# Kernel optimization log

Measured on AMD Instinct MI355X. Metric: run time of the kernel, lower is better.

Reference implementation:

```python
import jax, jax.numpy as jnp
import numpy as np

B, E, H, NF, NO, L = 1024, 256, 4, 16384, 49152, 192
DH = E // H
NEG = -1e9  # effectively -inf for masked-out padded keys


def _positions(batch, n, offset_counts=None):
    # batch is sorted; within-segment index = i - segment_start[batch[i]]
    counts = jax.ops.segment_sum(jnp.ones((n,), jnp.int32), batch, num_segments=B)
    start = jnp.cumsum(counts) - counts
    pos = jnp.arange(n, dtype=jnp.int32) - start[batch]
    if offset_counts is not None:
        pos = pos + offset_counts[batch]
    return pos, counts


def setup_inputs() -> dict:
    key = jax.random.key(0)
    ks = jax.random.split(key, 8)
    scene_feat = jax.random.normal(ks[0], (B, E), jnp.float32)
    face_nodes = jax.random.normal(ks[1], (NF, E), jnp.float32)
    obj_nodes = jax.random.normal(ks[2], (NO, E), jnp.float32)
    face_batch = jnp.sort(jax.random.randint(ks[3], (NF,), 0, B))
    obj_batch = jnp.sort(jax.random.randint(ks[4], (NO,), 0, B))
    s = 1.0 / np.sqrt(E)
    in_proj_w = jax.random.uniform(ks[5], (3 * E, E), jnp.float32, -s, s)
    in_proj_b = jnp.zeros((3 * E,), jnp.float32)
    out_proj_w = jax.random.uniform(ks[6], (E, E), jnp.float32, -s, s)
    out_proj_b = jnp.zeros((E,), jnp.float32)
    ln_gamma = jnp.ones((E,), jnp.float32)
    ln_beta = jnp.zeros((E,), jnp.float32)
    return dict(scene_feat=scene_feat, face_nodes=face_nodes, obj_nodes=obj_nodes,
                face_batch=face_batch, obj_batch=obj_batch,
                in_proj_w=in_proj_w, in_proj_b=in_proj_b,
                out_proj_w=out_proj_w, out_proj_b=out_proj_b,
                ln_gamma=ln_gamma, ln_beta=ln_beta)


def reference(scene_feat, face_nodes, obj_nodes, face_batch, obj_batch,
              in_proj_w, in_proj_b, out_proj_w, out_proj_b, ln_gamma, ln_beta):
    # --- to_dense_batch over concat([face, obj]) : faces first per graph ---
    pos_f, counts_f = _positions(face_batch, NF)
    pos_o, _ = _positions(obj_batch, NO, offset_counts=counts_f)
    all_nodes = jnp.concatenate([face_nodes, obj_nodes], axis=0)   # [N, E]
    all_batch = jnp.concatenate([face_batch, obj_batch], axis=0)   # [N]
    all_pos = jnp.concatenate([pos_f, pos_o], axis=0)              # [N]
    slot = jnp.where(all_pos < L, all_pos, L)                      # overflow -> sentinel col
    dense = jnp.zeros((B, L + 1, E), all_nodes.dtype).at[all_batch, slot].set(all_nodes)[:, :L]
    mask = jnp.zeros((B, L + 1), bool).at[all_batch, slot].set(True)[:, :L]

    # --- single-query multihead cross-attention (torch MHA semantics) ---
    wq, wk, wv = in_proj_w[:E], in_proj_w[E:2 * E], in_proj_w[2 * E:]
    bq, bk, bv = in_proj_b[:E], in_proj_b[E:2 * E], in_proj_b[2 * E:]
    q = (scene_feat @ wq.T + bq).reshape(B, H, DH)                 # [B,H,DH]
    k = (dense @ wk.T + bk).reshape(B, L, H, DH)
    v = (dense @ wv.T + bv).reshape(B, L, H, DH)
    scores = jnp.einsum('bhd,blhd->bhl', q, k) / np.sqrt(DH)        # [B,H,L]
    scores = jnp.where(mask[:, None, :], scores, NEG)
    attn = jax.nn.softmax(scores, axis=-1)                          # [B,H,L]
    ctx = jnp.einsum('bhl,blhd->bhd', attn, v).reshape(B, E)
    attn_out = ctx @ out_proj_w.T + out_proj_b                      # [B,E]

    # --- residual + LayerNorm ---
    x = scene_feat + attn_out
    mu = jnp.mean(x, axis=-1, keepdims=True)
    var = jnp.mean(jnp.square(x - mu), axis=-1, keepdims=True)
    fused = (x - mu) * jax.lax.rsqrt(var + 1e-5) * ln_gamma + ln_beta  # [B,E]

    attn_weights = jnp.mean(attn, axis=1)[:, None, :]               # [B,1,L] head-averaged
    return fused, attn_weights
```

## Files before the change

### kernel.cpp

```cpp
#include <hip/hip_runtime.h>
#include <math.h>

#define B 1024
#define E 256
#define H 4
#define DH 64
#define L 192
#define NF 16384
#define NO 49152
#define BPB 4

__global__ __launch_bounds__(256) void prep_kernel(
    const int* __restrict__ fb, const int* __restrict__ ob,
    int* __restrict__ start_f, int* __restrict__ start_o,
    const float* __restrict__ ipw, const float* __restrict__ opw,
    float* __restrict__ WT)
{
  int blk = blockIdx.x;
  if (blk < 192) {
    int m = blk / 64;
    int r = blk % 64;
    int bx = (r & 7) * 32, by = (r >> 3) * 32;
    const float* src = (m == 0) ? ipw : (m == 1 ? ipw + 2 * E * E : opw);
    float* dst = WT + (size_t)m * E * E;
    __shared__ float tile[32][33];
    int tx = threadIdx.x & 31, ty = threadIdx.x >> 5;
#pragma unroll
    for (int i = 0; i < 32; i += 8)
      tile[ty + i][tx] = src[(size_t)(by + ty + i) * E + bx + tx];
    __syncthreads();
#pragma unroll
    for (int i = 0; i < 32; i += 8)
      dst[(size_t)(bx + ty + i) * E + by + tx] = tile[tx][ty + i];
  } else {
    int b = (blk - 192) * 256 + threadIdx.x;
    if (b > B) return;
    int lo = 0, hi = NF;
    while (lo < hi) { int m = (lo + hi) >> 1; if (fb[m] < b) lo = m + 1; else hi = m; }
    start_f[b] = lo;
    lo = 0; hi = NO;
    while (lo < hi) { int m = (lo + hi) >> 1; if (ob[m] < b) lo = m + 1; else hi = m; }
    start_o[b] = lo;
  }
}

__global__ __launch_bounds__(512, 2) void fused_kernel(
    const float* __restrict__ scene,
    const float* __restrict__ face, const float* __restrict__ obj,
    const float* __restrict__ ipw, const float* __restrict__ ipb,
    const float* __restrict__ WqT, const float* __restrict__ WvT,
    const float* __restrict__ WoT, const float* __restrict__ opb,
    const float* __restrict__ gamma, const float* __restrict__ beta,
    const int* __restrict__ start_f, const int* __restrict__ start_o,
    float* __restrict__ fusedO, float* __restrict__ attnw)
{
  int b0 = blockIdx.x * BPB;
  int t = threadIdx.x, wave = t >> 6, lane = t & 63;

  __shared__ float sc_s[BPB][E];
  __shared__ float q_s[BPB][E];
  __shared__ float Y_s[BPB][H][E];
  __shared__ float Z_s[BPB][H][E];
  __shared__ float ctx_s[BPB][E];
  __shared__ float s_s[BPB][H][L];
  __shared__ float part_s[8][BPB][E];
  __shared__ float Zp_s[BPB][2][H][E];
  __shared__ float mw_s[BPB][2][H], su_s[BPB][2][H], sb_s[BPB][H];
  __shared__ int   info_s[BPB][4];

  for (int i = t; i < BPB * E; i += 512)
    ((float*)sc_s)[i] = scene[(size_t)b0 * E + i];
  if (t < BPB) {
    int b = b0 + t;
    int sf0 = start_f[b], cf = start_f[b + 1] - sf0;
    int so0 = start_o[b], co = start_o[b + 1] - so0;
    info_s[t][0] = sf0; info_s[t][1] = so0;
    info_s[t][2] = min(cf, L); info_s[t][3] = min(cf + co, L);
  }
  __syncthreads();

  {
    const float4* W4 = (const float4*)WqT + lane;
    float4 a0 = {0,0,0,0}, a1 = {0,0,0,0}, a2 = {0,0,0,0}, a3 = {0,0,0,0};
    int j0 = wave * 32;
#pragma unroll
    for (int jj = 0; jj < 32; ++jj) {
      int j = j0 + jj;
      float4 w = W4[(size_t)j * 64];
      float s0 = sc_s[0][j], s1 = sc_s[1][j], s2 = sc_s[2][j], s3 = sc_s[3][j];
      a0.x += s0*w.x; a0.y += s0*w.y; a0.z += s0*w.z; a0.w += s0*w.w;
      a1.x += s1*w.x; a1.y += s1*w.y; a1.z += s1*w.z; a1.w += s1*w.w;
      a2.x += s2*w.x; a2.y += s2*w.y; a2.z += s2*w.z; a2.w += s2*w.w;
      a3.x += s3*w.x; a3.y += s3*w.y; a3.z += s3*w.z; a3.w += s3*w.w;
    }
    *(float4*)&part_s[wave][0][4 * lane] = a0;
    *(float4*)&part_s[wave][1][4 * lane] = a1;
    *(float4*)&part_s[wave][2][4 * lane] = a2;
    *(float4*)&part_s[wave][3][4 * lane] = a3;
  }
  __syncthreads();
  for (int i = t; i < BPB * E; i += 512) {
    int bi = i >> 8, e = i & 255;
    float v = ipb[e];
#pragma unroll
    for (int w = 0; w < 8; ++w) v += part_s[w][bi][e];
    q_s[bi][e] = v;
  }
  __syncthreads();

  if (wave < BPB) {
#pragma unroll
    for (int h = 0; h < H; ++h) {
      float v = q_s[wave][h * DH + lane] * ipb[E + h * DH + lane];
#pragma unroll
      for (int o = 32; o; o >>= 1) v += __shfl_xor(v, o);
      if (lane == 0) sb_s[wave][h] = v;
    }
  }

  {
    const float* Wk = ipw + (size_t)E * E;
    int h = wave >> 1, d0 = (wave & 1) * 32;
    float4 a0 = {0,0,0,0}, a1 = {0,0,0,0}, a2 = {0,0,0,0}, a3 = {0,0,0,0};
#pragma unroll
    for (int dd = 0; dd < 32; ++dd) {
      int d = d0 + dd;
      float4 w = *((const float4*)(Wk + (size_t)(h * DH + d) * E) + lane);
      float q0 = q_s[0][h * DH + d], q1 = q_s[1][h * DH + d];
      float q2 = q_s[2][h * DH + d], q3 = q_s[3][h * DH + d];
      a0.x += q0*w.x; a0.y += q0*w.y; a0.z += q0*w.z; a0.w += q0*w.w;
      a1.x += q1*w.x; a1.y += q1*w.y; a1.z += q1*w.z; a1.w += q1*w.w;
      a2.x += q2*w.x; a2.y += q2*w.y; a2.z += q2*w.z; a2.w += q2*w.w;
      a3.x += q3*w.x; a3.y += q3*w.y; a3.z += q3*w.z; a3.w += q3*w.w;
    }
    float* Yp = (float*)part_s;
    int wi = wave & 1;
    size_t o0 = (((size_t)wi * BPB + 0) * H + h) * E + 4 * lane;
    size_t o1 = (((size_t)wi * BPB + 1) * H + h) * E + 4 * lane;
    size_t o2 = (((size_t)wi * BPB + 2) * H + h) * E + 4 * lane;
    size_t o3 = (((size_t)wi * BPB + 3) * H + h) * E + 4 * lane;
    *(float4*)&Yp[o0] = a0; *(float4*)&Yp[o1] = a1;
    *(float4*)&Yp[o2] = a2; *(float4*)&Yp[o3] = a3;
  }
  __syncthreads();
  {
    float* Yp = (float*)part_s;
    for (int i = t; i < BPB * H * E; i += 512)
      ((float*)Y_s)[i] = Yp[i] + Yp[BPB * H * E + i];
  }
  __syncthreads();

  {
    int bb = wave >> 1, wi = wave & 1;
    int g = lane >> 4, sl = lane & 15;
    int sf0 = info_s[bb][0], so0 = info_s[bb][1];
    int n_f = info_s[bb][2], n = info_s[bb][3];

    float4 y[H][4];
#pragma unroll
    for (int h = 0; h < H; ++h)
#pragma unroll
      for (int k = 0; k < 4; ++k)
        y[h][k] = *(const float4*)&Y_s[bb][h][4 * (sl + 16 * k)];
    float sbv[H];
#pragma unroll
    for (int h = 0; h < H; ++h) sbv[h] = sb_s[bb][h];

    float m[H] = {-3.0e38f, -3.0e38f, -3.0e38f, -3.0e38f};
    float u[H] = {0.f, 0.f, 0.f, 0.f};
    float4 acc[H][4] = {};

    int s0 = wi * 4 + g;
    float4 x[4] = {};
    if (s0 < n) {
      const float* xr = (s0 < n_f) ? face + (size_t)(sf0 + s0) * E
                                   : obj  + (size_t)(so0 + s0 - n_f) * E;
#pragma unroll
      for (int k = 0; k < 4; ++k) x[k] = ((const float4*)xr)[sl + 16 * k];
    }

    for (int s = s0; s < n; s += 8) {
      float4 xn[4] = {};
      int sn = s + 8;
      if (sn < n) {
        const float* xr = (sn < n_f) ? face + (size_t)(sf0 + sn) * E
                                     : obj  + (size_t)(so0 + sn - n_f) * E;
#pragma unroll
        for (int k = 0; k < 4; ++k) xn[k] = ((const float4*)xr)[sl + 16 * k];
      }

      float p[H];
#pragma unroll
      for (int h = 0; h < H; ++h) {
        float a = 0.f;
#pragma unroll
        for (int k = 0; k < 4; ++k)
          a += x[k].x * y[h][k].x + x[k].y * y[h][k].y +
               x[k].z * y[h][k].z + x[k].w * y[h][k].w;
        p[h] = a;
      }
#pragma unroll
      for (int off = 8; off; off >>= 1) {
#pragma unroll
        for (int h = 0; h < H; ++h) p[h] += __shfl_xor(p[h], off);
      }
#pragma unroll
      for (int h = 0; h < H; ++h) p[h] = (p[h] + sbv[h]) * 0.125f;
      if (sl == 0) {
#pragma unroll
        for (int h = 0; h < H; ++h) s_s[bb][h][s] = p[h];
      }
#pragma unroll
      for (int h = 0; h < H; ++h) {
        if (p[h] > m[h]) {
          float f = __expf(m[h] - p[h]);
#pragma unroll
          for (int k = 0; k < 4; ++k) {
            acc[h][k].x = acc[h][k].x * f + x[k].x;
            acc[h][k].y = acc[h][k].y * f + x[k].y;
            acc[h][k].z = acc[h][k].z * f + x[k].z;
            acc[h][k].w = acc[h][k].w * f + x[k].w;
          }
          u[h] = u[h] * f + 1.f;
          m[h] = p[h];
        } else {
          float e = __expf(p[h] - m[h]);
#pragma unroll
          for (int k = 0; k < 4; ++k) {
            acc[h][k].x += e * x[k].x;
            acc[h][k].y += e * x[k].y;
            acc[h][k].z += e * x[k].z;
            acc[h][k].w += e * x[k].w;
          }
          u[h] += e;
        }
      }
#pragma unroll
      for (int k = 0; k < 4; ++k) x[k] = xn[k];
    }

#pragma unroll
    for (int off = 16; off <= 32; off <<= 1) {
#pragma unroll
      for (int h = 0; h < H; ++h) {
        float mo = __shfl_xor(m[h], off);
        float uo = __shfl_xor(u[h], off);
        float M = fmaxf(m[h], mo);
        float fs = __expf(m[h] - M), fo = __expf(mo - M);
        u[h] = fs * u[h] + fo * uo;
        m[h] = M;
#pragma unroll
        for (int k = 0; k < 4; ++k) {
          float ax = __shfl_xor(acc[h][k].x, off);
          float ay = __shfl_xor(acc[h][k].y, off);
          float az = __shfl_xor(acc[h][k].z, off);
          float aw = __shfl_xor(acc[h][k].w, off);
          acc[h][k].x = fs * acc[h][k].x + fo * ax;
          acc[h][k].y = fs * acc[h][k].y + fo * ay;
          acc[h][k].z = fs * acc[h][k].z + fo * az;
          acc[h][k].w = fs * acc[h][k].w + fo * aw;
        }
      }
    }
    if (g == 0) {
#pragma unroll
      for (int h = 0; h < H; ++h)
#pragma unroll
        for (int k = 0; k < 4; ++k)
          *(float4*)&Zp_s[bb][wi][h][4 * (sl + 16 * k)] = acc[h][k];
    }
    if (lane == 0) {
#pragma unroll
      for (int h = 0; h < H; ++h) {
        mw_s[bb][wi][h] = m[h];
        su_s[bb][wi][h] = u[h];
      }
    }
  }
  __syncthreads();

  for (int i = t; i < BPB * H * E; i += 512) {
    int bi = i >> 10, rem = i & 1023, h = rem >> 8, e = rem & 255;
    float z = 0.f;
    if (info_s[bi][3] > 0) {
      float ma = mw_s[bi][0][h], mb = mw_s[bi][1][h];
      float M = fmaxf(ma, mb);
      float fa = __expf(ma - M), fb = __expf(mb - M);
      float inv = 1.0f / (fa * su_s[bi][0][h] + fb * su_s[bi][1][h]);
      z = (fa * Zp_s[bi][0][h][e] + fb * Zp_s[bi][1][h][e]) * inv;
    }
    ((float*)Z_s)[i] = z;
  }
  for (int i = t; i < BPB * L; i += 512) {
    int bi = i / L, s = i - bi * L;
    int n = info_s[bi][3];
    float v;
    if (n == 0) v = 1.0f / L;
    else if (s < n) {
      v = 0.f;
#pragma unroll
      for (int h = 0; h < H; ++h) {
        float ma = mw_s[bi][0][h], mb = mw_s[bi][1][h];
        float M = fmaxf(ma, mb);
        float fa = __expf(ma - M), fb = __expf(mb - M);
        float inv = 1.0f / (fa * su_s[bi][0][h] + fb * su_s[bi][1][h]);
        v += __expf(s_s[bi][h][s] - M) * inv;
      }
      v *= 0.25f;
    } else v = 0.f;
    attnw[(size_t)(b0 + bi) * L + s] = v;
  }
  __syncthreads();

  {
    const float4* W4 = (const float4*)WvT + lane;
    int j0 = wave * 32, hoff = (lane >> 4) * E;
    float4 a0 = {0,0,0,0}, a1 = {0,0,0,0}, a2 = {0,0,0,0}, a3 = {0,0,0,0};
#pragma unroll
    for (int jj = 0; jj < 32; ++jj) {
      int j = j0 + jj;
      float4 w = W4[(size_t)j * 64];
      float z0 = ((float*)Z_s[0])[hoff + j];
      float z1 = ((float*)Z_s[1])[hoff + j];
      float z2 = ((float*)Z_s[2])[hoff + j];
      float z3 = ((float*)Z_s[3])[hoff + j];
      a0.x += z0*w.x; a0.y += z0*w.y; a0.z += z0*w.z; a0.w += z0*w.w;
      a1.x += z1*w.x; a1.y += z1*w.y; a1.z += z1*w.z; a1.w += z1*w.w;
      a2.x += z2*w.x; a2.y += z2*w.y; a2.z += z2*w.z; a2.w += z2*w.w;
      a3.x += z3*w.x; a3.y += z3*w.y; a3.z += z3*w.z; a3.w += z3*w.w;
    }
    *(float4*)&part_s[wave][0][4 * lane] = a0;
    *(float4*)&part_s[wave][1][4 * lane] = a1;
    *(float4*)&part_s[wave][2][4 * lane] = a2;
    *(float4*)&part_s[wave][3][4 * lane] = a3;
  }
  __syncthreads();
  for (int i = t; i < BPB * E; i += 512) {
    int bi = i >> 8, e = i & 255;
    float v = ipb[2 * E + e];
#pragma unroll
    for (int w = 0; w < 8; ++w) v += part_s[w][bi][e];
    ctx_s[bi][e] = v;
  }
  __syncthreads();

  {
    const float4* W4 = (const float4*)WoT + lane;
    int j0 = wave * 32;
    float4 a0 = {0,0,0,0}, a1 = {0,0,0,0}, a2 = {0,0,0,0}, a3 = {0,0,0,0};
#pragma unroll
    for (int jj = 0; jj < 32; ++jj) {
      int j = j0 + jj;
      float4 w = W4[(size_t)j * 64];
      float c0 = ctx_s[0][j], c1 = ctx_s[1][j], c2 = ctx_s[2][j], c3 = ctx_s[3][j];
      a0.x += c0*w.x; a0.y += c0*w.y; a0.z += c0*w.z; a0.w += c0*w.w;
      a1.x += c1*w.x; a1.y += c1*w.y; a1.z += c1*w.z; a1.w += c1*w.w;
      a2.x += c2*w.x; a2.y += c2*w.y; a2.z += c2*w.z; a2.w += c2*w.w;
      a3.x += c3*w.x; a3.y += c3*w.y; a3.z += c3*w.z; a3.w += c3*w.w;
    }
    *(float4*)&part_s[wave][0][4 * lane] = a0;
    *(float4*)&part_s[wave][1][4 * lane] = a1;
    *(float4*)&part_s[wave][2][4 * lane] = a2;
    *(float4*)&part_s[wave][3][4 * lane] = a3;
  }
  __syncthreads();
  for (int i = t; i < BPB * E; i += 512) {
    int bi = i >> 8, e = i & 255;
    float v = opb[e] + sc_s[bi][e];
#pragma unroll
    for (int w = 0; w < 8; ++w) v += part_s[w][bi][e];
    q_s[bi][e] = v;
  }
  __syncthreads();

  if (wave < BPB) {
    float v0 = q_s[wave][lane], v1 = q_s[wave][lane + 64],
          v2 = q_s[wave][lane + 128], v3 = q_s[wave][lane + 192];
    float s1 = v0 + v1 + v2 + v3;
#pragma unroll
    for (int o = 32; o; o >>= 1) s1 += __shfl_xor(s1, o);
    float mu = s1 * (1.0f / E);
    float d0 = v0 - mu, d1 = v1 - mu, d2 = v2 - mu, d3 = v3 - mu;
    float s2 = d0*d0 + d1*d1 + d2*d2 + d3*d3;
#pragma unroll
    for (int o = 32; o; o >>= 1) s2 += __shfl_xor(s2, o);
    float inv = 1.0f / sqrtf(s2 * (1.0f / E) + 1e-5f);
    size_t base = (size_t)(b0 + wave) * E;
    fusedO[base + lane      ] = d0 * inv * gamma[lane      ] + beta[lane      ];
    fusedO[base + lane +  64] = d1 * inv * gamma[lane +  64] + beta[lane +  64];
    fusedO[base + lane + 128] = d2 * inv * gamma[lane + 128] + beta[lane + 128];
    fusedO[base + lane + 192] = d3 * inv * gamma[lane + 192] + beta[lane + 192];
  }
}

extern "C" void kernel_launch(void* const* d_in, const int* in_sizes, int n_in,
                              void* d_out, int out_size, void* d_ws, size_t ws_size,
                              hipStream_t stream) {
  const float* scene = (const float*)d_in[0];
  const float* face  = (const float*)d_in[1];
  const float* obj   = (const float*)d_in[2];
  const int*   fb    = (const int*)d_in[3];
  const int*   ob    = (const int*)d_in[4];
  const float* ipw   = (const float*)d_in[5];
  const float* ipb   = (const float*)d_in[6];
  const float* opw   = (const float*)d_in[7];
  const float* opb   = (const float*)d_in[8];
  const float* gam   = (const float*)d_in[9];
  const float* bet   = (const float*)d_in[10];

  float* fused = (float*)d_out;
  float* attnw = fused + (size_t)B * E;

  int* start_f = (int*)d_ws;
  int* start_o = start_f + (B + 1);
  float* WT   = (float*)((char*)d_ws + (16 << 10));
  float* WqT = WT;
  float* WvT = WT + (size_t)E * E;
  float* WoT = WT + (size_t)2 * E * E;

  prep_kernel<<<197, 256, 0, stream>>>(fb, ob, start_f, start_o, ipw, opw, WT);
  fused_kernel<<<B / BPB, 512, 0, stream>>>(scene, face, obj, ipw, ipb,
                                            WqT, WvT, WoT, opb, gam, bet,
                                            start_f, start_o, fused, attnw);
}
```

Before: 54.89 us.

## Split fused attention kernel into projection, per-batch streaming, and output kernels

The single fused kernel (4 batches per 512-thread block) is split into three kernels. qy_kernel computes q and the key-folded query Y. stream_kernel runs one 256-thread block per batch with 4 waves streaming that batch's node rows and merging their online-softmax partials. out_kernel applies the V and output projections plus LayerNorm. The aim is more parallelism in the memory-bound streaming phase, with four times as many blocks and smaller per-block shared memory, at the cost of two extra launches and global round-trips for Y and Z. The small GEMVs also drop their 4-batch register blocking, so each weight load is reused across fewer batches.

```diff
diff --git a/kernel.cpp b/kernel.cpp
--- a/kernel.cpp
+++ b/kernel.cpp
@@ -44,67 +44,42 @@
   }
 }
 
-__global__ __launch_bounds__(512, 2) void fused_kernel(
+__global__ __launch_bounds__(1024) void qy_kernel(
     const float* __restrict__ scene,
-    const float* __restrict__ face, const float* __restrict__ obj,
     const float* __restrict__ ipw, const float* __restrict__ ipb,
-    const float* __restrict__ WqT, const float* __restrict__ WvT,
-    const float* __restrict__ WoT, const float* __restrict__ opb,
-    const float* __restrict__ gamma, const float* __restrict__ beta,
-    const int* __restrict__ start_f, const int* __restrict__ start_o,
-    float* __restrict__ fusedO, float* __restrict__ attnw)
+    const float* __restrict__ WqT,
+    float* __restrict__ Yws, float* __restrict__ sbws)
 {
   int b0 = blockIdx.x * BPB;
   int t = threadIdx.x, wave = t >> 6, lane = t & 63;
+  int bw = wave >> 2, sub = wave & 3;
 
   __shared__ float sc_s[BPB][E];
   __shared__ float q_s[BPB][E];
-  __shared__ float Y_s[BPB][H][E];
-  __shared__ float Z_s[BPB][H][E];
-  __shared__ float ctx_s[BPB][E];
-  __shared__ float s_s[BPB][H][L];
-  __shared__ float part_s[8][BPB][E];
-  __shared__ float Zp_s[BPB][2][H][E];
-  __shared__ float mw_s[BPB][2][H], su_s[BPB][2][H], sb_s[BPB][H];
-  __shared__ int   info_s[BPB][4];
-
-  for (int i = t; i < BPB * E; i += 512)
-    ((float*)sc_s)[i] = scene[(size_t)b0 * E + i];
-  if (t < BPB) {
-    int b = b0 + t;
-    int sf0 = start_f[b], cf = start_f[b + 1] - sf0;
-    int so0 = start_o[b], co = start_o[b + 1] - so0;
-    info_s[t][0] = sf0; info_s[t][1] = so0;
-    info_s[t][2] = min(cf, L); info_s[t][3] = min(cf + co, L);
-  }
+  __shared__ float part_s[4][BPB][E];
+
+  sc_s[t >> 8][t & 255] = scene[(size_t)b0 * E + t];
   __syncthreads();
 
   {
     const float4* W4 = (const float4*)WqT + lane;
-    float4 a0 = {0,0,0,0}, a1 = {0,0,0,0}, a2 = {0,0,0,0}, a3 = {0,0,0,0};
-    int j0 = wave * 32;
-#pragma unroll
-    for (int jj = 0; jj < 32; ++jj) {
+    const float* sc = sc_s[bw];
+    float4 a = {0.f, 0.f, 0.f, 0.f};
+    int j0 = sub * 64;
+#pragma unroll 8
+    for (int jj = 0; jj < 64; ++jj) {
       int j = j0 + jj;
       float4 w = W4[(size_t)j * 64];
-      float s0 = sc_s[0][j], s1 = sc_s[1][j], s2 = sc_s[2][j], s3 = sc_s[3][j];
-      a0.x += s0*w.x; a0.y += s0*w.y; a0.z += s0*w.z; a0.w += s0*w.w;
-      a1.x += s1*w.x; a1.y += s1*w.y; a1.z += s1*w.z; a1.w += s1*w.w;
-      a2.x += s2*w.x; a2.y += s2*w.y; a2.z += s2*w.z; a2.w += s2*w.w;
-      a3.x += s3*w.x; a3.y += s3*w.y; a3.z += s3*w.z; a3.w += s3*w.w;
-    }
-    *(float4*)&part_s[wave][0][4 * lane] = a0;
-    *(float4*)&part_s[wave][1][4 * lane] = a1;
-    *(float4*)&part_s[wave][2][4 * lane] = a2;
-    *(float4*)&part_s[wave][3][4 * lane] = a3;
-  }
-  __syncthreads();
-  for (int i = t; i < BPB * E; i += 512) {
-    int bi = i >> 8, e = i & 255;
-    float v = ipb[e];
-#pragma unroll
-    for (int w = 0; w < 8; ++w) v += part_s[w][bi][e];
-    q_s[bi][e] = v;
+      float s = sc[j];
+      a.x += s * w.x; a.y += s * w.y; a.z += s * w.z; a.w += s * w.w;
+    }
+    *(float4*)&part_s[sub][bw][4 * lane] = a;
+  }
+  __syncthreads();
+  {
+    int bi = t >> 8, e = t & 255;
+    q_s[bi][e] = part_s[0][bi][e] + part_s[1][bi][e] +
+                 part_s[2][bi][e] + part_s[3][bi][e] + ipb[e];
   }
   __syncthreads();
 
@@ -114,268 +89,276 @@
       float v = q_s[wave][h * DH + lane] * ipb[E + h * DH + lane];
 #pragma unroll
       for (int o = 32; o; o >>= 1) v += __shfl_xor(v, o);
-      if (lane == 0) sb_s[wave][h] = v;
+      if (lane == 0) sbws[(size_t)(b0 + wave) * H + h] = v;
     }
   }
 
   {
     const float* Wk = ipw + (size_t)E * E;
-    int h = wave >> 1, d0 = (wave & 1) * 32;
-    float4 a0 = {0,0,0,0}, a1 = {0,0,0,0}, a2 = {0,0,0,0}, a3 = {0,0,0,0};
-#pragma unroll
-    for (int dd = 0; dd < 32; ++dd) {
-      int d = d0 + dd;
-      float4 w = *((const float4*)(Wk + (size_t)(h * DH + d) * E) + lane);
-      float q0 = q_s[0][h * DH + d], q1 = q_s[1][h * DH + d];
-      float q2 = q_s[2][h * DH + d], q3 = q_s[3][h * DH + d];
-      a0.x += q0*w.x; a0.y += q0*w.y; a0.z += q0*w.z; a0.w += q0*w.w;
-      a1.x += q1*w.x; a1.y += q1*w.y; a1.z += q1*w.z; a1.w += q1*w.w;
-      a2.x += q2*w.x; a2.y += q2*w.y; a2.z += q2*w.z; a2.w += q2*w.w;
-      a3.x += q3*w.x; a3.y += q3*w.y; a3.z += q3*w.z; a3.w += q3*w.w;
-    }
-    float* Yp = (float*)part_s;
-    int wi = wave & 1;
-    size_t o0 = (((size_t)wi * BPB + 0) * H + h) * E + 4 * lane;
-    size_t o1 = (((size_t)wi * BPB + 1) * H + h) * E + 4 * lane;
-    size_t o2 = (((size_t)wi * BPB + 2) * H + h) * E + 4 * lane;
-    size_t o3 = (((size_t)wi * BPB + 3) * H + h) * E + 4 * lane;
-    *(float4*)&Yp[o0] = a0; *(float4*)&Yp[o1] = a1;
-    *(float4*)&Yp[o2] = a2; *(float4*)&Yp[o3] = a3;
-  }
-  __syncthreads();
-  {
-    float* Yp = (float*)part_s;
-    for (int i = t; i < BPB * H * E; i += 512)
-      ((float*)Y_s)[i] = Yp[i] + Yp[BPB * H * E + i];
-  }
-  __syncthreads();
-
-  {
-    int bb = wave >> 1, wi = wave & 1;
-    int g = lane >> 4, sl = lane & 15;
-    int sf0 = info_s[bb][0], so0 = info_s[bb][1];
-    int n_f = info_s[bb][2], n = info_s[bb][3];
-
-    float4 y[H][4];
+    float4 a = {0.f, 0.f, 0.f, 0.f};
+#pragma unroll 8
+    for (int d = 0; d < DH; ++d) {
+      float qv = q_s[bw][sub * DH + d];
+      float4 w = *((const float4*)(Wk + (size_t)(sub * DH + d) * E) + lane);
+      a.x += qv * w.x; a.y += qv * w.y; a.z += qv * w.z; a.w += qv * w.w;
+    }
+    *(float4*)&Yws[((size_t)(b0 + bw) * H + sub) * E + 4 * lane] = a;
+  }
+}
+
+__global__ __launch_bounds__(256, 4) void stream_kernel(
+    const float* __restrict__ face, const float* __restrict__ obj,
+    const float* __restrict__ Yws, const float* __restrict__ sbws,
+    const int* __restrict__ start_f, const int* __restrict__ start_o,
+    float* __restrict__ Zws, float* __restrict__ attnw)
+{
+  int b = blockIdx.x, t = threadIdx.x;
+  int wave = t >> 6, lane = t & 63;
+  int g = lane >> 4, sl = lane & 15;
+
+  __shared__ float Y_s[H][E];
+  __shared__ float s_s[H][L];
+  __shared__ float Zp_s[4][H][E];
+  __shared__ float mw_s[4][H], su_s[4][H], sb_s[H];
+
+  int sf0 = start_f[b], cf = start_f[b + 1] - sf0;
+  int so0 = start_o[b], co = start_o[b + 1] - so0;
+  int n_f = min(cf, L);
+  int n   = min(cf + co, L);
+
+  for (int i = t; i < H * E; i += 256)
+    ((float*)Y_s)[i] = Yws[(size_t)b * (H * E) + i];
+  if (t < H) sb_s[t] = sbws[(size_t)b * H + t];
+  __syncthreads();
+
+  float4 y[H][4];
+#pragma unroll
+  for (int h = 0; h < H; ++h)
+#pragma unroll
+    for (int k = 0; k < 4; ++k)
+      y[h][k] = *(const float4*)&Y_s[h][4 * (sl + 16 * k)];
+  float sbv[H];
+#pragma unroll
+  for (int h = 0; h < H; ++h) sbv[h] = sb_s[h];
+
+  float m[H] = {-3.0e38f, -3.0e38f, -3.0e38f, -3.0e38f};
+  float u[H] = {0.f, 0.f, 0.f, 0.f};
+  float4 acc[H][4] = {};
+
+  int s0 = wave * 4 + g;
+  float4 x[4] = {};
+  if (s0 < n) {
+    const float* xr = (s0 < n_f) ? face + (size_t)(sf0 + s0) * E
+                                 : obj  + (size_t)(so0 + s0 - n_f) * E;
+#pragma unroll
+    for (int k = 0; k < 4; ++k) x[k] = ((const float4*)xr)[sl + 16 * k];
+  }
+
+  for (int s = s0; s < n; s += 16) {
+    float4 xn[4] = {};
+    int sn = s + 16;
+    if (sn < n) {
+      const float* xr = (sn < n_f) ? face + (size_t)(sf0 + sn) * E
+                                   : obj  + (size_t)(so0 + sn - n_f) * E;
+#pragma unroll
+      for (int k = 0; k < 4; ++k) xn[k] = ((const float4*)xr)[sl + 16 * k];
+    }
+
+    float p[H];
+#pragma unroll
+    for (int h = 0; h < H; ++h) {
+      float a = 0.f;
+#pragma unroll
+      for (int k = 0; k < 4; ++k)
+        a += x[k].x * y[h][k].x + x[k].y * y[h][k].y +
+             x[k].z * y[h][k].z + x[k].w * y[h][k].w;
+      p[h] = a;
+    }
+#pragma unroll
+    for (int off = 8; off; off >>= 1) {
+#pragma unroll
+      for (int h = 0; h < H; ++h) p[h] += __shfl_xor(p[h], off);
+    }
+#pragma unroll
+    for (int h = 0; h < H; ++h) p[h] = (p[h] + sbv[h]) * 0.125f;
+    if (sl == 0) {
+#pragma unroll
+      for (int h = 0; h < H; ++h) s_s[h][s] = p[h];
+    }
+#pragma unroll
+    for (int h = 0; h < H; ++h) {
+      if (p[h] > m[h]) {
+        float f = __expf(m[h] - p[h]);
+#pragma unroll
+        for (int k = 0; k < 4; ++k) {
+          acc[h][k].x = acc[h][k].x * f + x[k].x;
+          acc[h][k].y = acc[h][k].y * f + x[k].y;
+          acc[h][k].z = acc[h][k].z * f + x[k].z;
+          acc[h][k].w = acc[h][k].w * f + x[k].w;
+        }
+        u[h] = u[h] * f + 1.f;
+        m[h] = p[h];
+      } else {
+        float e = __expf(p[h] - m[h]);
+#pragma unroll
+        for (int k = 0; k < 4; ++k) {
+          acc[h][k].x += e * x[k].x;
+          acc[h][k].y += e * x[k].y;
+          acc[h][k].z += e * x[k].z;
+          acc[h][k].w += e * x[k].w;
+        }
+        u[h] += e;
+      }
+    }
+#pragma unroll
+    for (int k = 0; k < 4; ++k) x[k] = xn[k];
+  }
+
+#pragma unroll
+  for (int off = 16; off <= 32; off <<= 1) {
+#pragma unroll
+    for (int h = 0; h < H; ++h) {
+      float mo = __shfl_xor(m[h], off);
+      float uo = __shfl_xor(u[h], off);
+      float M = fmaxf(m[h], mo);
+      float fs = __expf(m[h] - M), fo = __expf(mo - M);
+      u[h] = fs * u[h] + fo * uo;
+      m[h] = M;
+#pragma unroll
+      for (int k = 0; k < 4; ++k) {
+        float ax = __shfl_xor(acc[h][k].x, off);
+        float ay = __shfl_xor(acc[h][k].y, off);
+        float az = __shfl_xor(acc[h][k].z, off);
+        float aw = __shfl_xor(acc[h][k].w, off);
+        acc[h][k].x = fs * acc[h][k].x + fo * ax;
+        acc[h][k].y = fs * acc[h][k].y + fo * ay;
+        acc[h][k].z = fs * acc[h][k].z + fo * az;
+        acc[h][k].w = fs * acc[h][k].w + fo * aw;
+      }
+    }
+  }
+  if (g == 0) {
 #pragma unroll
     for (int h = 0; h < H; ++h)
 #pragma unroll
       for (int k = 0; k < 4; ++k)
-        y[h][k] = *(const float4*)&Y_s[bb][h][4 * (sl + 16 * k)];
-    float sbv[H];
-#pragma unroll
-    for (int h = 0; h < H; ++h) sbv[h] = sb_s[bb][h];
-
-    float m[H] = {-3.0e38f, -3.0e38f, -3.0e38f, -3.0e38f};
-    float u[H] = {0.f, 0.f, 0.f, 0.f};
-    float4 acc[H][4] = {};
-
-    int s0 = wi * 4 + g;
-    float4 x[4] = {};
-    if (s0 < n) {
-      const float* xr = (s0 < n_f) ? face + (size_t)(sf0 + s0) * E
-                                   : obj  + (size_t)(so0 + s0 - n_f) * E;
-#pragma unroll
-      for (int k = 0; k < 4; ++k) x[k] = ((const float4*)xr)[sl + 16 * k];
-    }
-
-    for (int s = s0; s < n; s += 8) {
-      float4 xn[4] = {};
-      int sn = s + 8;
-      if (sn < n) {
-        const float* xr = (sn < n_f) ? face + (size_t)(sf0 + sn) * E
-                                     : obj  + (size_t)(so0 + sn - n_f) * E;
-#pragma unroll
-        for (int k = 0; k < 4; ++k) xn[k] = ((const float4*)xr)[sl + 16 * k];
-      }
-
-      float p[H];
-#pragma unroll
-      for (int h = 0; h < H; ++h) {
-        float a = 0.f;
-#pragma unroll
-        for (int k = 0; k < 4; ++k)
-          a += x[k].x * y[h][k].x + x[k].y * y[h][k].y +
-               x[k].z * y[h][k].z + x[k].w * y[h][k].w;
-        p[h] = a;
-      }
-#pragma unroll
-      for (int off = 8; off; off >>= 1) {
-#pragma unroll
-        for (int h = 0; h < H; ++h) p[h] += __shfl_xor(p[h], off);
-      }
-#pragma unroll
-      for (int h = 0; h < H; ++h) p[h] = (p[h] + sbv[h]) * 0.125f;
-      if (sl == 0) {
-#pragma unroll
-        for (int h = 0; h < H; ++h) s_s[bb][h][s] = p[h];
-      }
-#pragma unroll
-      for (int h = 0; h < H; ++h) {
-        if (p[h] > m[h]) {
-          float f = __expf(m[h] - p[h]);
-#pragma unroll
-          for (int k = 0; k < 4; ++k) {
-            acc[h][k].x = acc[h][k].x * f + x[k].x;
-            acc[h][k].y = acc[h][k].y * f + x[k].y;
-            acc[h][k].z = acc[h][k].z * f + x[k].z;
-            acc[h][k].w = acc[h][k].w * f + x[k].w;
-          }
-          u[h] = u[h] * f + 1.f;
-          m[h] = p[h];
-        } else {
-          float e = __expf(p[h] - m[h]);
-#pragma unroll
-          for (int k = 0; k < 4; ++k) {
-            acc[h][k].x += e * x[k].x;
-            acc[h][k].y += e * x[k].y;
-            acc[h][k].z += e * x[k].z;
-            acc[h][k].w += e * x[k].w;
-          }
-          u[h] += e;
-        }
-      }
-#pragma unroll
-      for (int k = 0; k < 4; ++k) x[k] = xn[k];
-    }
-
-#pragma unroll
-    for (int off = 16; off <= 32; off <<= 1) {
-#pragma unroll
-      for (int h = 0; h < H; ++h) {
-        float mo = __shfl_xor(m[h], off);
-        float uo = __shfl_xor(u[h], off);
-        float M = fmaxf(m[h], mo);
-        float fs = __expf(m[h] - M), fo = __expf(mo - M);
-        u[h] = fs * u[h] + fo * uo;
-        m[h] = M;
-#pragma unroll
-        for (int k = 0; k < 4; ++k) {
-          float ax = __shfl_xor(acc[h][k].x, off);
-          float ay = __shfl_xor(acc[h][k].y, off);
-          float az = __shfl_xor(acc[h][k].z, off);
-          float aw = __shfl_xor(acc[h][k].w, off);
-          acc[h][k].x = fs * acc[h][k].x + fo * ax;
-          acc[h][k].y = fs * acc[h][k].y + fo * ay;
-          acc[h][k].z = fs * acc[h][k].z + fo * az;
-          acc[h][k].w = fs * acc[h][k].w + fo * aw;
-        }
-      }
-    }
-    if (g == 0) {
-#pragma unroll
-      for (int h = 0; h < H; ++h)
-#pragma unroll
-        for (int k = 0; k < 4; ++k)
-          *(float4*)&Zp_s[bb][wi][h][4 * (sl + 16 * k)] = acc[h][k];
-    }
-    if (lane == 0) {
-#pragma unroll
-      for (int h = 0; h < H; ++h) {
-        mw_s[bb][wi][h] = m[h];
-        su_s[bb][wi][h] = u[h];
-      }
-    }
-  }
-  __syncthreads();
-
-  for (int i = t; i < BPB * H * E; i += 512) {
-    int bi = i >> 10, rem = i & 1023, h = rem >> 8, e = rem & 255;
+        *(float4*)&Zp_s[wave][h][4 * (sl + 16 * k)] = acc[h][k];
+  }
+  if (lane == 0) {
+#pragma unroll
+    for (int h = 0; h < H; ++h) {
+      mw_s[wave][h] = m[h];
+      su_s[wave][h] = u[h];
+    }
+  }
+  __syncthreads();
+
+  for (int i = t; i < H * E; i += 256) {
+    int h = i >> 8, e = i & 255;
     float z = 0.f;
-    if (info_s[bi][3] > 0) {
-      float ma = mw_s[bi][0][h], mb = mw_s[bi][1][h];
-      float M = fmaxf(ma, mb);
+    if (n > 0) {
+      float ma = mw_s[0][h], mb = mw_s[1][h], mc = mw_s[2][h], md = mw_s[3][h];
+      float M = fmaxf(fmaxf(ma, mb), fmaxf(mc, md));
       float fa = __expf(ma - M), fb = __expf(mb - M);
-      float inv = 1.0f / (fa * su_s[bi][0][h] + fb * su_s[bi][1][h]);
-      z = (fa * Zp_s[bi][0][h][e] + fb * Zp_s[bi][1][h][e]) * inv;
-    }
-    ((float*)Z_s)[i] = z;
-  }
-  for (int i = t; i < BPB * L; i += 512) {
-    int bi = i / L, s = i - bi * L;
-    int n = info_s[bi][3];
+      float fc = __expf(mc - M), fd = __expf(md - M);
+      float inv = 1.0f / (fa * su_s[0][h] + fb * su_s[1][h] +
+                          fc * su_s[2][h] + fd * su_s[3][h]);
+      z = (fa * Zp_s[0][h][e] + fb * Zp_s[1][h][e] +
+           fc * Zp_s[2][h][e] + fd * Zp_s[3][h][e]) * inv;
+    }
+    Zws[(size_t)b * (H * E) + i] = z;
+  }
+  if (t < L) {
     float v;
     if (n == 0) v = 1.0f / L;
-    else if (s < n) {
+    else if (t < n) {
       v = 0.f;
 #pragma unroll
       for (int h = 0; h < H; ++h) {
-        float ma = mw_s[bi][0][h], mb = mw_s[bi][1][h];
-        float M = fmaxf(ma, mb);
+        float ma = mw_s[0][h], mb = mw_s[1][h], mc = mw_s[2][h], md = mw_s[3][h];
+        float M = fmaxf(fmaxf(ma, mb), fmaxf(mc, md));
         float fa = __expf(ma - M), fb = __expf(mb - M);
-        float inv = 1.0f / (fa * su_s[bi][0][h] + fb * su_s[bi][1][h]);
-        v += __expf(s_s[bi][h][s] - M) * inv;
+        float fc = __expf(mc - M), fd = __expf(md - M);
+        float inv = 1.0f / (fa * su_s[0][h] + fb * su_s[1][h] +
+                            fc * su_s[2][h] + fd * su_s[3][h]);
+        v += __expf(s_s[h][t] - M) * inv;
       }
       v *= 0.25f;
     } else v = 0.f;
-    attnw[(size_t)(b0 + bi) * L + s] = v;
-  }
+    attnw[(size_t)b * L + t] = v;
+  }
+}
+
+__global__ __launch_bounds__(1024) void out_kernel(
+    const float* __restrict__ scene, const float* __restrict__ Zws,
+    const float* __restrict__ ipb,
+    const float* __restrict__ WvT, const float* __restrict__ WoT,
+    const float* __restrict__ opb,
+    const float* __restrict__ gamma, const float* __restrict__ beta,
+    float* __restrict__ fusedO)
+{
+  int b0 = blockIdx.x * BPB;
+  int t = threadIdx.x, wave = t >> 6, lane = t & 63;
+  int bw = wave >> 2, sub = wave & 3;
+
+  __shared__ float Z_s[BPB][H * E];
+  __shared__ float sc_s[BPB][E];
+  __shared__ float ctx_s[BPB][E];
+  __shared__ float x_s[BPB][E];
+  __shared__ float part_s[4][BPB][E];
+
+  for (int i = t; i < BPB * H * E; i += 1024)
+    ((float*)Z_s)[i] = Zws[(size_t)b0 * (H * E) + i];
+  sc_s[t >> 8][t & 255] = scene[(size_t)b0 * E + t];
   __syncthreads();
 
   {
     const float4* W4 = (const float4*)WvT + lane;
-    int j0 = wave * 32, hoff = (lane >> 4) * E;
-    float4 a0 = {0,0,0,0}, a1 = {0,0,0,0}, a2 = {0,0,0,0}, a3 = {0,0,0,0};
-#pragma unroll
-    for (int jj = 0; jj < 32; ++jj) {
+    const float* zr = Z_s[bw] + (lane >> 4) * E;
+    float4 a = {0.f, 0.f, 0.f, 0.f};
+    int j0 = sub * 64;
+#pragma unroll 8
+    for (int jj = 0; jj < 64; ++jj) {
       int j = j0 + jj;
       float4 w = W4[(size_t)j * 64];
-      float z0 = ((float*)Z_s[0])[hoff + j];
-      float z1 = ((float*)Z_s[1])[hoff + j];
-      float z2 = ((float*)Z_s[2])[hoff + j];
-      float z3 = ((float*)Z_s[3])[hoff + j];
-      a0.x += z0*w.x; a0.y += z0*w.y; a0.z += z0*w.z; a0.w += z0*w.w;
-      a1.x += z1*w.x; a1.y += z1*w.y; a1.z += z1*w.z; a1.w += z1*w.w;
-      a2.x += z2*w.x; a2.y += z2*w.y; a2.z += z2*w.z; a2.w += z2*w.w;
-      a3.x += z3*w.x; a3.y += z3*w.y; a3.z += z3*w.z; a3.w += z3*w.w;
-    }
-    *(float4*)&part_s[wave][0][4 * lane] = a0;
-    *(float4*)&part_s[wave][1][4 * lane] = a1;
-    *(float4*)&part_s[wave][2][4 * lane] = a2;
-    *(float4*)&part_s[wave][3][4 * lane] = a3;
-  }
-  __syncthreads();
-  for (int i = t; i < BPB * E; i += 512) {
-    int bi = i >> 8, e = i & 255;
-    float v = ipb[2 * E + e];
-#pragma unroll
-    for (int w = 0; w < 8; ++w) v += part_s[w][bi][e];
-    ctx_s[bi][e] = v;
+      float zv = zr[j];
+      a.x += zv * w.x; a.y += zv * w.y; a.z += zv * w.z; a.w += zv * w.w;
+    }
+    *(float4*)&part_s[sub][bw][4 * lane] = a;
+  }
+  __syncthreads();
+  {
+    int bi = t >> 8, e = t & 255;
+    ctx_s[bi][e] = part_s[0][bi][e] + part_s[1][bi][e] +
+                   part_s[2][bi][e] + part_s[3][bi][e] + ipb[2 * E + e];
   }
   __syncthreads();
 
   {
     const float4* W4 = (const float4*)WoT + lane;
-    int j0 = wave * 32;
-    float4 a0 = {0,0,0,0}, a1 = {0,0,0,0}, a2 = {0,0,0,0}, a3 = {0,0,0,0};
-#pragma unroll
-    for (int jj = 0; jj < 32; ++jj) {
+    const float* cr = ctx_s[bw];
+    float4 a = {0.f, 0.f, 0.f, 0.f};
+    int j0 = sub * 64;
+#pragma unroll 8
+    for (int jj = 0; jj < 64; ++jj) {
       int j = j0 + jj;
       float4 w = W4[(size_t)j * 64];
-      float c0 = ctx_s[0][j], c1 = ctx_s[1][j], c2 = ctx_s[2][j], c3 = ctx_s[3][j];
-      a0.x += c0*w.x; a0.y += c0*w.y; a0.z += c0*w.z; a0.w += c0*w.w;
-      a1.x += c1*w.x; a1.y += c1*w.y; a1.z += c1*w.z; a1.w += c1*w.w;
-      a2.x += c2*w.x; a2.y += c2*w.y; a2.z += c2*w.z; a2.w += c2*w.w;
-      a3.x += c3*w.x; a3.y += c3*w.y; a3.z += c3*w.z; a3.w += c3*w.w;
-    }
-    *(float4*)&part_s[wave][0][4 * lane] = a0;
-    *(float4*)&part_s[wave][1][4 * lane] = a1;
-    *(float4*)&part_s[wave][2][4 * lane] = a2;
-    *(float4*)&part_s[wave][3][4 * lane] = a3;
-  }
-  __syncthreads();
-  for (int i = t; i < BPB * E; i += 512) {
-    int bi = i >> 8, e = i & 255;
-    float v = opb[e] + sc_s[bi][e];
-#pragma unroll
-    for (int w = 0; w < 8; ++w) v += part_s[w][bi][e];
-    q_s[bi][e] = v;
+      float cv = cr[j];
+      a.x += cv * w.x; a.y += cv * w.y; a.z += cv * w.z; a.w += cv * w.w;
+    }
+    *(float4*)&part_s[sub][bw][4 * lane] = a;
+  }
+  __syncthreads();
+  {
+    int bi = t >> 8, e = t & 255;
+    x_s[bi][e] = part_s[0][bi][e] + part_s[1][bi][e] +
+                 part_s[2][bi][e] + part_s[3][bi][e] + opb[e] + sc_s[bi][e];
   }
   __syncthreads();
 
   if (wave < BPB) {
-    float v0 = q_s[wave][lane], v1 = q_s[wave][lane + 64],
-          v2 = q_s[wave][lane + 128], v3 = q_s[wave][lane + 192];
+    float v0 = x_s[wave][lane], v1 = x_s[wave][lane + 64],
+          v2 = x_s[wave][lane + 128], v3 = x_s[wave][lane + 192];
     float s1 = v0 + v1 + v2 + v3;
 #pragma unroll
     for (int o = 32; o; o >>= 1) s1 += __shfl_xor(s1, o);
@@ -414,12 +397,15 @@
   int* start_f = (int*)d_ws;
   int* start_o = start_f + (B + 1);
   float* WT   = (float*)((char*)d_ws + (16 << 10));
-  float* WqT = WT;
-  float* WvT = WT + (size_t)E * E;
-  float* WoT = WT + (size_t)2 * E * E;
+  float* WqT  = WT;
+  float* WvT  = WT + (size_t)E * E;
+  float* WoT  = WT + (size_t)2 * E * E;
+  float* Yws  = WT + (size_t)3 * E * E;
+  float* sbws = Yws + (size_t)B * H * E;
+  float* Zws  = sbws + (size_t)B * H + 4096;
 
   prep_kernel<<<197, 256, 0, stream>>>(fb, ob, start_f, start_o, ipw, opw, WT);
-  fused_kernel<<<B / BPB, 512, 0, stream>>>(scene, face, obj, ipw, ipb,
-                                            WqT, WvT, WoT, opb, gam, bet,
-                                            start_f, start_o, fused, attnw);
+  qy_kernel<<<B / BPB, 1024, 0, stream>>>(scene, ipw, ipb, WqT, Yws, sbws);
+  stream_kernel<<<B, 256, 0, stream>>>(face, obj, Yws, sbws, start_f, start_o, Zws, attnw);
+  out_kernel<<<B / BPB, 1024, 0, stream>>>(scene, Zws, ipb, WvT, WoT, opb, gam, bet, fused);
 }
```

Result: slower. 188.7 us (+243.8%).

## Split attention heads across waves and overlay shared buffers for higher occupancy

Applied to the files above, without the earlier changes.

The attention loop now gives each wave two heads across all keys of a graph, instead of all four heads over half the keys. This removes the cross-wave softmax merge and halves the per-thread accumulator registers. The Y/Z and partial-sum buffers are merged into one reused shared array, shrinking LDS so launch bounds can request four blocks per CU. In exchange, every wave now reads all key rows, so each row is loaded twice (once per head pair), and the loop runs twice as many iterations per wave.

```diff
diff --git a/kernel.cpp b/kernel.cpp
--- a/kernel.cpp
+++ b/kernel.cpp
@@ -44,7 +44,7 @@
   }
 }
 
-__global__ __launch_bounds__(512, 2) void fused_kernel(
+__global__ __launch_bounds__(512, 4) void fused_kernel(
     const float* __restrict__ scene,
     const float* __restrict__ face, const float* __restrict__ obj,
     const float* __restrict__ ipw, const float* __restrict__ ipb,
@@ -59,13 +59,11 @@
 
   __shared__ float sc_s[BPB][E];
   __shared__ float q_s[BPB][E];
-  __shared__ float Y_s[BPB][H][E];
-  __shared__ float Z_s[BPB][H][E];
+  __shared__ float YZ_s[BPB][H][E];
   __shared__ float ctx_s[BPB][E];
   __shared__ float s_s[BPB][H][L];
-  __shared__ float part_s[8][BPB][E];
-  __shared__ float Zp_s[BPB][2][H][E];
-  __shared__ float mw_s[BPB][2][H], su_s[BPB][2][H], sb_s[BPB][H];
+  __shared__ float un_s[8192];
+  __shared__ float mw_s[BPB][2][2], su_s[BPB][2][2], sb_s[BPB][H];
   __shared__ int   info_s[BPB][4];
 
   for (int i = t; i < BPB * E; i += 512)
@@ -93,17 +91,17 @@
       a2.x += s2*w.x; a2.y += s2*w.y; a2.z += s2*w.z; a2.w += s2*w.w;
       a3.x += s3*w.x; a3.y += s3*w.y; a3.z += s3*w.z; a3.w += s3*w.w;
     }
-    *(float4*)&part_s[wave][0][4 * lane] = a0;
-    *(float4*)&part_s[wave][1][4 * lane] = a1;
-    *(float4*)&part_s[wave][2][4 * lane] = a2;
-    *(float4*)&part_s[wave][3][4 * lane] = a3;
+    *(float4*)&un_s[((wave * BPB + 0) << 8) + 4 * lane] = a0;
+    *(float4*)&un_s[((wave * BPB + 1) << 8) + 4 * lane] = a1;
+    *(float4*)&un_s[((wave * BPB + 2) << 8) + 4 * lane] = a2;
+    *(float4*)&un_s[((wave * BPB + 3) << 8) + 4 * lane] = a3;
   }
   __syncthreads();
   for (int i = t; i < BPB * E; i += 512) {
     int bi = i >> 8, e = i & 255;
     float v = ipb[e];
 #pragma unroll
-    for (int w = 0; w < 8; ++w) v += part_s[w][bi][e];
+    for (int w = 0; w < 8; ++w) v += un_s[((w * BPB + bi) << 8) + e];
     q_s[bi][e] = v;
   }
   __syncthreads();
@@ -120,7 +118,7 @@
 
   {
     const float* Wk = ipw + (size_t)E * E;
-    int h = wave >> 1, d0 = (wave & 1) * 32;
+    int h = wave >> 1, d0 = (wave & 1) * 32, wi = wave & 1;
     float4 a0 = {0,0,0,0}, a1 = {0,0,0,0}, a2 = {0,0,0,0}, a3 = {0,0,0,0};
 #pragma unroll
     for (int dd = 0; dd < 32; ++dd) {
@@ -133,55 +131,45 @@
       a2.x += q2*w.x; a2.y += q2*w.y; a2.z += q2*w.z; a2.w += q2*w.w;
       a3.x += q3*w.x; a3.y += q3*w.y; a3.z += q3*w.z; a3.w += q3*w.w;
     }
-    float* Yp = (float*)part_s;
-    int wi = wave & 1;
-    size_t o0 = (((size_t)wi * BPB + 0) * H + h) * E + 4 * lane;
-    size_t o1 = (((size_t)wi * BPB + 1) * H + h) * E + 4 * lane;
-    size_t o2 = (((size_t)wi * BPB + 2) * H + h) * E + 4 * lane;
-    size_t o3 = (((size_t)wi * BPB + 3) * H + h) * E + 4 * lane;
-    *(float4*)&Yp[o0] = a0; *(float4*)&Yp[o1] = a1;
-    *(float4*)&Yp[o2] = a2; *(float4*)&Yp[o3] = a3;
-  }
-  __syncthreads();
+    *(float4*)&un_s[wi * 4096 + ((0 * H + h) << 8) + 4 * lane] = a0;
+    *(float4*)&un_s[wi * 4096 + ((1 * H + h) << 8) + 4 * lane] = a1;
+    *(float4*)&un_s[wi * 4096 + ((2 * H + h) << 8) + 4 * lane] = a2;
+    *(float4*)&un_s[wi * 4096 + ((3 * H + h) << 8) + 4 * lane] = a3;
+  }
+  __syncthreads();
+  for (int i = t; i < BPB * H * E; i += 512)
+    ((float*)YZ_s)[i] = un_s[i] + un_s[4096 + i];
+  __syncthreads();
+
   {
-    float* Yp = (float*)part_s;
-    for (int i = t; i < BPB * H * E; i += 512)
-      ((float*)Y_s)[i] = Yp[i] + Yp[BPB * H * E + i];
-  }
-  __syncthreads();
-
-  {
-    int bb = wave >> 1, wi = wave & 1;
+    int bb = wave >> 1, hp = wave & 1, h0 = hp * 2;
     int g = lane >> 4, sl = lane & 15;
     int sf0 = info_s[bb][0], so0 = info_s[bb][1];
     int n_f = info_s[bb][2], n = info_s[bb][3];
 
-    float4 y[H][4];
-#pragma unroll
-    for (int h = 0; h < H; ++h)
+    float4 y[2][4];
+#pragma unroll
+    for (int hh = 0; hh < 2; ++hh)
 #pragma unroll
       for (int k = 0; k < 4; ++k)
-        y[h][k] = *(const float4*)&Y_s[bb][h][4 * (sl + 16 * k)];
-    float sbv[H];
-#pragma unroll
-    for (int h = 0; h < H; ++h) sbv[h] = sb_s[bb][h];
-
-    float m[H] = {-3.0e38f, -3.0e38f, -3.0e38f, -3.0e38f};
-    float u[H] = {0.f, 0.f, 0.f, 0.f};
-    float4 acc[H][4] = {};
-
-    int s0 = wi * 4 + g;
+        y[hh][k] = *(const float4*)&YZ_s[bb][h0 + hh][4 * (sl + 16 * k)];
+    float sbv[2] = {sb_s[bb][h0], sb_s[bb][h0 + 1]};
+
+    float m[2] = {-3.0e38f, -3.0e38f};
+    float u[2] = {0.f, 0.f};
+    float4 acc[2][4] = {};
+
     float4 x[4] = {};
-    if (s0 < n) {
-      const float* xr = (s0 < n_f) ? face + (size_t)(sf0 + s0) * E
-                                   : obj  + (size_t)(so0 + s0 - n_f) * E;
+    if (g < n) {
+      const float* xr = (g < n_f) ? face + (size_t)(sf0 + g) * E
+                                  : obj  + (size_t)(so0 + g - n_f) * E;
 #pragma unroll
       for (int k = 0; k < 4; ++k) x[k] = ((const float4*)xr)[sl + 16 * k];
     }
 
-    for (int s = s0; s < n; s += 8) {
+    for (int s = g; s < n; s += 4) {
       float4 xn[4] = {};
-      int sn = s + 8;
+      int sn = s + 4;
       if (sn < n) {
         const float* xr = (sn < n_f) ? face + (size_t)(sf0 + sn) * E
                                      : obj  + (size_t)(so0 + sn - n_f) * E;
@@ -189,50 +177,50 @@
         for (int k = 0; k < 4; ++k) xn[k] = ((const float4*)xr)[sl + 16 * k];
       }
 
-      float p[H];
-#pragma unroll
-      for (int h = 0; h < H; ++h) {
+      float p[2];
+#pragma unroll
+      for (int hh = 0; hh < 2; ++hh) {
         float a = 0.f;
 #pragma unroll
         for (int k = 0; k < 4; ++k)
-          a += x[k].x * y[h][k].x + x[k].y * y[h][k].y +
-               x[k].z * y[h][k].z + x[k].w * y[h][k].w;
-        p[h] = a;
+          a += x[k].x * y[hh][k].x + x[k].y * y[hh][k].y +
+               x[k].z * y[hh][k].z + x[k].w * y[hh][k].w;
+        p[hh] = a;
       }
 #pragma unroll
       for (int off = 8; off; off >>= 1) {
-#pragma unroll
-        for (int h = 0; h < H; ++h) p[h] += __shfl_xor(p[h], off);
-      }
-#pragma unroll
-      for (int h = 0; h < H; ++h) p[h] = (p[h] + sbv[h]) * 0.125f;
+        p[0] += __shfl_xor(p[0], off);
+        p[1] += __shfl_xor(p[1], off);
+      }
+      p[0] = (p[0] + sbv[0]) * 0.125f;
+      p[1] = (p[1] + sbv[1]) * 0.125f;
       if (sl == 0) {
-#pragma unroll
-        for (int h = 0; h < H; ++h) s_s[bb][h][s] = p[h];
-      }
-#pragma unroll
-      for (int h = 0; h < H; ++h) {
-        if (p[h] > m[h]) {
-          float f = __expf(m[h] - p[h]);
+        s_s[bb][h0][s] = p[0];
+        s_s[bb][h0 + 1][s] = p[1];
+      }
+#pragma unroll
+      for (int hh = 0; hh < 2; ++hh) {
+        if (p[hh] > m[hh]) {
+          float f = __expf(m[hh] - p[hh]);
 #pragma unroll
           for (int k = 0; k < 4; ++k) {
-            acc[h][k].x = acc[h][k].x * f + x[k].x;
-            acc[h][k].y = acc[h][k].y * f + x[k].y;
-            acc[h][k].z = acc[h][k].z * f + x[k].z;
-            acc[h][k].w = acc[h][k].w * f + x[k].w;
+            acc[hh][k].x = acc[hh][k].x * f + x[k].x;
+            acc[hh][k].y = acc[hh][k].y * f + x[k].y;
+            acc[hh][k].z = acc[hh][k].z * f + x[k].z;
+            acc[hh][k].w = acc[hh][k].w * f + x[k].w;
           }
-          u[h] = u[h] * f + 1.f;
-          m[h] = p[h];
+          u[hh] = u[hh] * f + 1.f;
+          m[hh] = p[hh];
         } else {
-          float e = __expf(p[h] - m[h]);
+          float e = __expf(p[hh] - m[hh]);
 #pragma unroll
           for (int k = 0; k < 4; ++k) {
-            acc[h][k].x += e * x[k].x;
-            acc[h][k].y += e * x[k].y;
-            acc[h][k].z += e * x[k].z;
-            acc[h][k].w += e * x[k].w;
+            acc[hh][k].x += e * x[k].x;
+            acc[hh][k].y += e * x[k].y;
+            acc[hh][k].z += e * x[k].z;
+            acc[hh][k].w += e * x[k].w;
           }
-          u[h] += e;
+          u[hh] += e;
         }
       }
 #pragma unroll
@@ -242,39 +230,36 @@
 #pragma unroll
     for (int off = 16; off <= 32; off <<= 1) {
 #pragma unroll
-      for (int h = 0; h < H; ++h) {
-        float mo = __shfl_xor(m[h], off);
-        float uo = __shfl_xor(u[h], off);
-        float M = fmaxf(m[h], mo);
-        float fs = __expf(m[h] - M), fo = __expf(mo - M);
-        u[h] = fs * u[h] + fo * uo;
-        m[h] = M;
+      for (int hh = 0; hh < 2; ++hh) {
+        float mo = __shfl_xor(m[hh], off);
+        float uo = __shfl_xor(u[hh], off);
+        float M = fmaxf(m[hh], mo);
+        float fs = __expf(m[hh] - M), fo = __expf(mo - M);
+        u[hh] = fs * u[hh] + fo * uo;
+        m[hh] = M;
 #pragma unroll
         for (int k = 0; k < 4; ++k) {
-          float ax = __shfl_xor(acc[h][k].x, off);
-          float ay = __shfl_xor(acc[h][k].y, off);
-          float az = __shfl_xor(acc[h][k].z, off);
-          float aw = __shfl_xor(acc[h][k].w, off);
-          acc[h][k].x = fs * acc[h][k].x + fo * ax;
-          acc[h][k].y = fs * acc[h][k].y + fo * ay;
-          acc[h][k].z = fs * acc[h][k].z + fo * az;
-          acc[h][k].w = fs * acc[h][k].w + fo * aw;
+          float ax = __shfl_xor(acc[hh][k].x, off);
+          float ay = __shfl_xor(acc[hh][k].y, off);
+          float az = __shfl_xor(acc[hh][k].z, off);
+          float aw = __shfl_xor(acc[hh][k].w, off);
+          acc[hh][k].x = fs * acc[hh][k].x + fo * ax;
+          acc[hh][k].y = fs * acc[hh][k].y + fo * ay;
+          acc[hh][k].z = fs * acc[hh][k].z + fo * az;
+          acc[hh][k].w = fs * acc[hh][k].w + fo * aw;
         }
       }
     }
     if (g == 0) {
 #pragma unroll
-      for (int h = 0; h < H; ++h)
+      for (int hh = 0; hh < 2; ++hh)
 #pragma unroll
         for (int k = 0; k < 4; ++k)
-          *(float4*)&Zp_s[bb][wi][h][4 * (sl + 16 * k)] = acc[h][k];
+          *(float4*)&un_s[(((bb * 2 + hp) * 2 + hh) << 8) + 4 * (sl + 16 * k)] = acc[hh][k];
     }
     if (lane == 0) {
-#pragma unroll
-      for (int h = 0; h < H; ++h) {
-        mw_s[bb][wi][h] = m[h];
-        su_s[bb][wi][h] = u[h];
-      }
+      mw_s[bb][hp][0] = m[0]; mw_s[bb][hp][1] = m[1];
+      su_s[bb][hp][0] = u[0]; su_s[bb][hp][1] = u[1];
     }
   }
   __syncthreads();
@@ -283,13 +268,11 @@
     int bi = i >> 10, rem = i & 1023, h = rem >> 8, e = rem & 255;
     float z = 0.f;
     if (info_s[bi][3] > 0) {
-      float ma = mw_s[bi][0][h], mb = mw_s[bi][1][h];
-      float M = fmaxf(ma, mb);
-      float fa = __expf(ma - M), fb = __expf(mb - M);
-      float inv = 1.0f / (fa * su_s[bi][0][h] + fb * su_s[bi][1][h]);
-      z = (fa * Zp_s[bi][0][h][e] + fb * Zp_s[bi][1][h][e]) * inv;
-    }
-    ((float*)Z_s)[i] = z;
+      int hp = h >> 1, hh = h & 1;
+      float inv = 1.0f / su_s[bi][hp][hh];
+      z = un_s[(((bi * 2 + hp) * 2 + hh) << 8) + e] * inv;
+    }
+    ((float*)YZ_s)[i] = z;
   }
   for (int i = t; i < BPB * L; i += 512) {
     int bi = i / L, s = i - bi * L;
@@ -300,11 +283,8 @@
       v = 0.f;
 #pragma unroll
       for (int h = 0; h < H; ++h) {
-        float ma = mw_s[bi][0][h], mb = mw_s[bi][1][h];
-        float M = fmaxf(ma, mb);
-        float fa = __expf(ma - M), fb = __expf(mb - M);
-        float inv = 1.0f / (fa * su_s[bi][0][h] + fb * su_s[bi][1][h]);
-        v += __expf(s_s[bi][h][s] - M) * inv;
+        int hp = h >> 1, hh = h & 1;
+        v += __expf(s_s[bi][h][s] - mw_s[bi][hp][hh]) / su_s[bi][hp][hh];
       }
       v *= 0.25f;
     } else v = 0.f;
@@ -320,26 +300,26 @@
     for (int jj = 0; jj < 32; ++jj) {
       int j = j0 + jj;
       float4 w = W4[(size_t)j * 64];
-      float z0 = ((float*)Z_s[0])[hoff + j];
-      float z1 = ((float*)Z_s[1])[hoff + j];
-      float z2 = ((float*)Z_s[2])[hoff + j];
-      float z3 = ((float*)Z_s[3])[hoff + j];
+      float z0 = ((float*)YZ_s[0])[hoff + j];
+      float z1 = ((float*)YZ_s[1])[hoff + j];
+      float z2 = ((float*)YZ_s[2])[hoff + j];
+      float z3 = ((float*)YZ_s[3])[hoff + j];
       a0.x += z0*w.x; a0.y += z0*w.y; a0.z += z0*w.z; a0.w += z0*w.w;
       a1.x += z1*w.x; a1.y += z1*w.y; a1.z += z1*w.z; a1.w += z1*w.w;
       a2.x += z2*w.x; a2.y += z2*w.y; a2.z += z2*w.z; a2.w += z2*w.w;
       a3.x += z3*w.x; a3.y += z3*w.y; a3.z += z3*w.z; a3.w += z3*w.w;
     }
-    *(float4*)&part_s[wave][0][4 * lane] = a0;
-    *(float4*)&part_s[wave][1][4 * lane] = a1;
-    *(float4*)&part_s[wave][2][4 * lane] = a2;
-    *(float4*)&part_s[wave][3][4 * lane] = a3;
+    *(float4*)&un_s[((wave * BPB + 0) << 8) + 4 * lane] = a0;
+    *(float4*)&un_s[((wave * BPB + 1) << 8) + 4 * lane] = a1;
+    *(float4*)&un_s[((wave * BPB + 2) << 8) + 4 * lane] = a2;
+    *(float4*)&un_s[((wave * BPB + 3) << 8) + 4 * lane] = a3;
   }
   __syncthreads();
   for (int i = t; i < BPB * E; i += 512) {
     int bi = i >> 8, e = i & 255;
     float v = ipb[2 * E + e];
 #pragma unroll
-    for (int w = 0; w < 8; ++w) v += part_s[w][bi][e];
+    for (int w = 0; w < 8; ++w) v += un_s[((w * BPB + bi) << 8) + e];
     ctx_s[bi][e] = v;
   }
   __syncthreads();
@@ -358,17 +338,17 @@
       a2.x += c2*w.x; a2.y += c2*w.y; a2.z += c2*w.z; a2.w += c2*w.w;
       a3.x += c3*w.x; a3.y += c3*w.y; a3.z += c3*w.z; a3.w += c3*w.w;
     }
-    *(float4*)&part_s[wave][0][4 * lane] = a0;
-    *(float4*)&part_s[wave][1][4 * lane] = a1;
-    *(float4*)&part_s[wave][2][4 * lane] = a2;
-    *(float4*)&part_s[wave][3][4 * lane] = a3;
+    *(float4*)&un_s[((wave * BPB + 0) << 8) + 4 * lane] = a0;
+    *(float4*)&un_s[((wave * BPB + 1) << 8) + 4 * lane] = a1;
+    *(float4*)&un_s[((wave * BPB + 2) << 8) + 4 * lane] = a2;
+    *(float4*)&un_s[((wave * BPB + 3) << 8) + 4 * lane] = a3;
   }
   __syncthreads();
   for (int i = t; i < BPB * E; i += 512) {
     int bi = i >> 8, e = i & 255;
     float v = opb[e] + sc_s[bi][e];
 #pragma unroll
-    for (int w = 0; w < 8; ++w) v += part_s[w][bi][e];
+    for (int w = 0; w < 8; ++w) v += un_s[((w * BPB + bi) << 8) + e];
     q_s[bi][e] = v;
   }
   __syncthreads();
```

Result: slower. 56.93 us (+3.7%).
